# Kernel optimization log

Measured on AMD Instinct MI355X. Metric: run time of the kernel, lower is better.

The kernel has to match this reference:

```python
import jax, jax.numpy as jnp
import numpy as np

N, M, D = 1024, 1024, 256


def setup_inputs() -> dict:
    key = jax.random.key(0)
    k1, k2 = jax.random.split(key)
    z_x = jax.random.normal(k1, (N, D), dtype=jnp.float32)
    z_y = jax.random.normal(k2, (M, D), dtype=jnp.float32)
    return {"z_x": z_x, "z_y": z_y}


def reference(z_x, z_y):
    # s[i, j] = -sum_d |z_x[i, d] - z_y[j, d]|   -> [N, M] negative L1 distances
    s = -jnp.sum(jnp.abs(z_x[:, None, :] - z_y[None, :, :]), axis=-1)
    a = jax.nn.softmax(s, axis=1)  # row-wise alignment probs
    b = jax.nn.softmax(s, axis=0)  # column-wise alignment probs
    w = a + b - a * b              # soft symmetric alignment weights
    # weighted mean similarity (scalar)
    c = jnp.sum(w * s) / jnp.sum(w)
    return c
```

## Files before the change

### kernel.cpp

```cpp
#include <hip/hip_runtime.h>
#include <math.h>

#define NN 1024
#define MM 1024
#define DD 256
#define TI 32
#define TJ 64
#define NTI 32
#define NTJ 16
#define PITCH_H 264

typedef _Float16 f16x2 __attribute__((ext_vector_type(2)));
typedef _Float16 f16x4 __attribute__((ext_vector_type(4)));

__device__ inline f16x2 habs2(f16x2 v) {
  unsigned u = __builtin_bit_cast(unsigned, v) & 0x7FFF7FFFu;
  return __builtin_bit_cast(f16x2, u);
}

__device__ inline float dot2acc(f16x2 a, float acc) {
#if __has_builtin(__builtin_amdgcn_fdot2)
  const f16x2 one = {(_Float16)1.0f, (_Float16)1.0f};
  return __builtin_amdgcn_fdot2(a, one, acc, false);
#else
  return acc + (float)a.x + (float)a.y;
#endif
}

__device__ inline void merge_ms(float& m, float& s, float m2, float s2) {
  float mn = fmaxf(m, m2);
  s = s * __expf(m - mn) + s2 * __expf(m2 - mn);
  m = mn;
}

__device__ inline float wredSum(float v) {
#pragma unroll
  for (int o = 32; o > 0; o >>= 1) v += __shfl_down(v, o, 64);
  return v;
}

__global__ __launch_bounds__(256) void k_tile(const float* __restrict__ zx,
                                              const float* __restrict__ zy,
                                              float* __restrict__ S,
                                              float* __restrict__ rowPM,
                                              float* __restrict__ rowPS,
                                              float* __restrict__ colPM,
                                              float* __restrict__ colPS) {
  __shared__ __align__(16) _Float16 xs[TI * PITCH_H];
  __shared__ __align__(16) _Float16 ys[TJ * PITCH_H];
  __shared__ float lm[16][64];
  __shared__ float lsv[16][64];

  const int it = blockIdx.y, jt = blockIdx.x;
  const int i0 = it * TI, j0 = jt * TJ;
  const int t = threadIdx.x;
  const int tx = t & 15, ty = t >> 4;

#pragma unroll
  for (int k = 0; k < 8; ++k) {
    int idx4 = t + k * 256;
    int r = idx4 >> 6;
    int c4 = idx4 & 63;
    float4 v = reinterpret_cast<const float4*>(zx + (size_t)(i0 + r) * DD)[c4];
    f16x4 h = {(_Float16)v.x, (_Float16)v.y, (_Float16)v.z, (_Float16)v.w};
    *reinterpret_cast<f16x4*>(&xs[r * PITCH_H + c4 * 4]) = h;
  }
#pragma unroll
  for (int k = 0; k < 16; ++k) {
    int idx4 = t + k * 256;
    int r = idx4 >> 6;
    int c4 = idx4 & 63;
    float4 v = reinterpret_cast<const float4*>(zy + (size_t)(j0 + r) * DD)[c4];
    f16x4 h = {(_Float16)v.x, (_Float16)v.y, (_Float16)v.z, (_Float16)v.w};
    *reinterpret_cast<f16x4*>(&ys[r * PITCH_H + c4 * 4]) = h;
  }
  __syncthreads();

  float acc4[2][4] = {{0.f}};
  for (int s8 = 0; s8 < 32; ++s8) {
    uint4 xw[2], yw[4];
#pragma unroll
    for (int a = 0; a < 2; ++a)
      xw[a] = *reinterpret_cast<const uint4*>(&xs[(ty + a * 16) * PITCH_H + s8 * 8]);
#pragma unroll
    for (int b = 0; b < 4; ++b)
      yw[b] = *reinterpret_cast<const uint4*>(&ys[(tx + b * 16) * PITCH_H + s8 * 8]);
#pragma unroll
    for (int a = 0; a < 2; ++a)
#pragma unroll
      for (int b = 0; b < 4; ++b) {
        float acc = acc4[a][b];
        acc = dot2acc(habs2(__builtin_bit_cast(f16x2, xw[a].x) - __builtin_bit_cast(f16x2, yw[b].x)), acc);
        acc = dot2acc(habs2(__builtin_bit_cast(f16x2, xw[a].y) - __builtin_bit_cast(f16x2, yw[b].y)), acc);
        acc = dot2acc(habs2(__builtin_bit_cast(f16x2, xw[a].z) - __builtin_bit_cast(f16x2, yw[b].z)), acc);
        acc = dot2acc(habs2(__builtin_bit_cast(f16x2, xw[a].w) - __builtin_bit_cast(f16x2, yw[b].w)), acc);
        acc4[a][b] = acc;
      }
  }

#pragma unroll
  for (int a = 0; a < 2; ++a) {
    int i = i0 + ty + a * 16;
#pragma unroll
    for (int b = 0; b < 4; ++b) {
      int j = j0 + tx + b * 16;
      S[(size_t)i * MM + j] = -acc4[a][b];
    }
  }

#pragma unroll
  for (int a = 0; a < 2; ++a) {
    float m = -acc4[a][0];
#pragma unroll
    for (int b = 1; b < 4; ++b) m = fmaxf(m, -acc4[a][b]);
    float s = 0.f;
#pragma unroll
    for (int b = 0; b < 4; ++b) s += __expf(-acc4[a][b] - m);
#pragma unroll
    for (int off = 1; off < 16; off <<= 1) {
      float m2 = __shfl_xor(m, off, 64);
      float s2 = __shfl_xor(s, off, 64);
      merge_ms(m, s, m2, s2);
    }
    if (tx == 0) {
      int i = i0 + ty + a * 16;
      rowPM[(size_t)jt * NN + i] = m;
      rowPS[(size_t)jt * NN + i] = s;
    }
  }

#pragma unroll
  for (int b = 0; b < 4; ++b) {
    int c = tx + b * 16;
    float m = fmaxf(-acc4[0][b], -acc4[1][b]);
    float s = __expf(-acc4[0][b] - m) + __expf(-acc4[1][b] - m);
    lm[ty][c] = m;
    lsv[ty][c] = s;
  }
  __syncthreads();
  if (t < 64) {
    float m = lm[0][t], s = lsv[0][t];
#pragma unroll
    for (int k = 1; k < 16; ++k) merge_ms(m, s, lm[k][t], lsv[k][t]);
    colPM[(size_t)it * MM + j0 + t] = m;
    colPS[(size_t)it * MM + j0 + t] = s;
  }
}

__global__ __launch_bounds__(256) void k_merge(const float* __restrict__ rowPM,
                                               const float* __restrict__ rowPS,
                                               const float* __restrict__ colPM,
                                               const float* __restrict__ colPS,
                                               float* __restrict__ rowM,
                                               float* __restrict__ rowS,
                                               float* __restrict__ colM,
                                               float* __restrict__ colS) {
  int g = blockIdx.x * 256 + threadIdx.x;
  if (g < NN) {
    float m = rowPM[g], s = rowPS[g];
#pragma unroll
    for (int k = 1; k < NTJ; ++k)
      merge_ms(m, s, rowPM[(size_t)k * NN + g], rowPS[(size_t)k * NN + g]);
    rowM[g] = m;
    rowS[g] = s;
  } else {
    int c = g - NN;
    float m = colPM[c], s = colPS[c];
#pragma unroll
    for (int k = 1; k < NTI; ++k)
      merge_ms(m, s, colPM[(size_t)k * MM + c], colPS[(size_t)k * MM + c]);
    colM[c] = m;
    colS[c] = s;
  }
}

__global__ __launch_bounds__(256) void k_accum(const float* __restrict__ S,
                                               const float* __restrict__ rowM,
                                               const float* __restrict__ rowS,
                                               const float* __restrict__ colM,
                                               const float* __restrict__ colS,
                                               float* __restrict__ bNum,
                                               float* __restrict__ bDen) {
  const int i = blockIdx.x;
  const int t = threadIdx.x;
  float4 v = reinterpret_cast<const float4*>(S + (size_t)i * MM)[t];
  const float rm = rowM[i];
  const float rinv = 1.f / rowS[i];
  float4 cm = reinterpret_cast<const float4*>(colM)[t];
  float4 cs = reinterpret_cast<const float4*>(colS)[t];
  float num = 0.f, den = 0.f;
#define DO_COMP(VX, CMX, CSX)               \
  {                                         \
    float a = __expf((VX) - rm) * rinv;     \
    float b = __expf((VX) - (CMX)) / (CSX); \
    float w = a + b - a * b;                \
    num += w * (VX);                        \
    den += w;                               \
  }
  DO_COMP(v.x, cm.x, cs.x)
  DO_COMP(v.y, cm.y, cs.y)
  DO_COMP(v.z, cm.z, cs.z)
  DO_COMP(v.w, cm.w, cs.w)
#undef DO_COMP
  num = wredSum(num);
  den = wredSum(den);
  __shared__ float rn[4], rd[4];
  const int lane = t & 63, wv = t >> 6;
  if (lane == 0) { rn[wv] = num; rd[wv] = den; }
  __syncthreads();
  if (t == 0) {
    bNum[i] = rn[0] + rn[1] + rn[2] + rn[3];
    bDen[i] = rd[0] + rd[1] + rd[2] + rd[3];
  }
}

__global__ __launch_bounds__(256) void k_final(const float* __restrict__ bNum,
                                               const float* __restrict__ bDen,
                                               float* __restrict__ out) {
  const int t = threadIdx.x;
  float4 n4 = reinterpret_cast<const float4*>(bNum)[t];
  float4 d4 = reinterpret_cast<const float4*>(bDen)[t];
  float n = n4.x + n4.y + n4.z + n4.w;
  float d = d4.x + d4.y + d4.z + d4.w;
  n = wredSum(n);
  d = wredSum(d);
  __shared__ float rn[4], rd[4];
  const int lane = t & 63, wv = t >> 6;
  if (lane == 0) { rn[wv] = n; rd[wv] = d; }
  __syncthreads();
  if (t == 0) out[0] = (rn[0] + rn[1] + rn[2] + rn[3]) / (rd[0] + rd[1] + rd[2] + rd[3]);
}

extern "C" void kernel_launch(void* const* d_in, const int* in_sizes, int n_in,
                              void* d_out, int out_size, void* d_ws, size_t ws_size,
                              hipStream_t stream) {
  const float* zx = (const float*)d_in[0];
  const float* zy = (const float*)d_in[1];
  float* out = (float*)d_out;

  float* ws = (float*)d_ws;
  float* S     = ws;
  float* rowPM = S + (size_t)NN * MM;
  float* rowPS = rowPM + NTJ * NN;
  float* colPM = rowPS + NTJ * NN;
  float* colPS = colPM + NTI * MM;
  float* rowM  = colPS + NTI * MM;
  float* rowS  = rowM + NN;
  float* colM  = rowS + NN;
  float* colS  = colM + MM;
  float* bNum  = colS + MM;
  float* bDen  = bNum + NN;

  k_tile<<<dim3(NTJ, NTI), 256, 0, stream>>>(zx, zy, S, rowPM, rowPS, colPM, colPS);
  k_merge<<<8, 256, 0, stream>>>(rowPM, rowPS, colPM, colPS, rowM, rowS, colM, colS);
  k_accum<<<NN, 256, 0, stream>>>(S, rowM, rowS, colM, colS, bNum, bDen);
  k_final<<<1, 256, 0, stream>>>(bNum, bDen, out);
}
```

Measured before the change: 32.30 us.

## Fold merge and final reduction into tile and accum kernels via last-block atomics

Removes the separate merge and final-reduction kernels. The last tile block to finish a row or column strip, detected with atomic counters, now merges the partial max and sum statistics. The last accumulation block reduces the per-block sums to the scalar output. The accumulation kernel now handles four rows per block and precomputes the column reciprocals. This cuts two kernel launches and their gaps, at the cost of counters that are never reset (they rely on modular wraparound) and extra fences.

```diff
diff --git a/kernel.cpp b/kernel.cpp
--- a/kernel.cpp
+++ b/kernel.cpp
@@ -45,7 +45,13 @@
                                               float* __restrict__ rowPM,
                                               float* __restrict__ rowPS,
                                               float* __restrict__ colPM,
-                                              float* __restrict__ colPS) {
+                                              float* __restrict__ colPS,
+                                              float* __restrict__ rowM,
+                                              float* __restrict__ rowS,
+                                              float* __restrict__ colM,
+                                              float* __restrict__ colS,
+                                              unsigned* __restrict__ rowCtr,
+                                              unsigned* __restrict__ colCtr) {
   __shared__ __align__(16) _Float16 xs[TI * PITCH_H];
   __shared__ __align__(16) _Float16 ys[TJ * PITCH_H];
   __shared__ float lm[16][64];
@@ -145,32 +151,40 @@
     colPM[(size_t)it * MM + j0 + t] = m;
     colPS[(size_t)it * MM + j0 + t] = s;
   }
-}
-
-__global__ __launch_bounds__(256) void k_merge(const float* __restrict__ rowPM,
-                                               const float* __restrict__ rowPS,
-                                               const float* __restrict__ colPM,
-                                               const float* __restrict__ colPS,
-                                               float* __restrict__ rowM,
-                                               float* __restrict__ rowS,
-                                               float* __restrict__ colM,
-                                               float* __restrict__ colS) {
-  int g = blockIdx.x * 256 + threadIdx.x;
-  if (g < NN) {
-    float m = rowPM[g], s = rowPS[g];
-#pragma unroll
-    for (int k = 1; k < NTJ; ++k)
-      merge_ms(m, s, rowPM[(size_t)k * NN + g], rowPS[(size_t)k * NN + g]);
-    rowM[g] = m;
-    rowS[g] = s;
-  } else {
-    int c = g - NN;
-    float m = colPM[c], s = colPS[c];
-#pragma unroll
-    for (int k = 1; k < NTI; ++k)
-      merge_ms(m, s, colPM[(size_t)k * MM + c], colPS[(size_t)k * MM + c]);
-    colM[c] = m;
-    colS[c] = s;
+
+  __syncthreads();
+  __shared__ int doRow, doCol;
+  if (t == 0) {
+    __threadfence();
+    unsigned o1 = atomicAdd(&rowCtr[it], 1u);
+    doRow = ((o1 & (NTJ - 1u)) == (NTJ - 1u)) ? 1 : 0;
+    unsigned o2 = atomicAdd(&colCtr[jt], 1u);
+    doCol = ((o2 & (NTI - 1u)) == (NTI - 1u)) ? 1 : 0;
+  }
+  __syncthreads();
+  if (doRow) {
+    __threadfence();
+    if (t < TI) {
+      int i = i0 + t;
+      float m = rowPM[i], s = rowPS[i];
+#pragma unroll
+      for (int k = 1; k < NTJ; ++k)
+        merge_ms(m, s, rowPM[(size_t)k * NN + i], rowPS[(size_t)k * NN + i]);
+      rowM[i] = m;
+      rowS[i] = s;
+    }
+  }
+  if (doCol) {
+    __threadfence();
+    if (t < TJ) {
+      int j = j0 + t;
+      float m = colPM[j], s = colPS[j];
+#pragma unroll
+      for (int k = 1; k < NTI; ++k)
+        merge_ms(m, s, colPM[(size_t)k * MM + j], colPS[(size_t)k * MM + j]);
+      colM[j] = m;
+      colS[j] = s;
+    }
   }
 }
 
@@ -180,28 +194,46 @@
                                                const float* __restrict__ colM,
                                                const float* __restrict__ colS,
                                                float* __restrict__ bNum,
-                                               float* __restrict__ bDen) {
-  const int i = blockIdx.x;
+                                               float* __restrict__ bDen,
+                                               unsigned* __restrict__ accCtr,
+                                               float* __restrict__ out) {
+  const int bid = blockIdx.x;
   const int t = threadIdx.x;
-  float4 v = reinterpret_cast<const float4*>(S + (size_t)i * MM)[t];
-  const float rm = rowM[i];
-  const float rinv = 1.f / rowS[i];
+
   float4 cm = reinterpret_cast<const float4*>(colM)[t];
   float4 cs = reinterpret_cast<const float4*>(colS)[t];
+  float4 ci;
+  ci.x = 1.f / cs.x; ci.y = 1.f / cs.y; ci.z = 1.f / cs.z; ci.w = 1.f / cs.w;
+
+  __shared__ float rowMl[4], rowIl[4];
+  if (t < 4) {
+    int r = bid * 4 + t;
+    rowMl[t] = rowM[r];
+    rowIl[t] = 1.f / rowS[r];
+  }
+  __syncthreads();
+
   float num = 0.f, den = 0.f;
-#define DO_COMP(VX, CMX, CSX)               \
-  {                                         \
-    float a = __expf((VX) - rm) * rinv;     \
-    float b = __expf((VX) - (CMX)) / (CSX); \
-    float w = a + b - a * b;                \
-    num += w * (VX);                        \
-    den += w;                               \
-  }
-  DO_COMP(v.x, cm.x, cs.x)
-  DO_COMP(v.y, cm.y, cs.y)
-  DO_COMP(v.z, cm.z, cs.z)
-  DO_COMP(v.w, cm.w, cs.w)
+#pragma unroll
+  for (int rl = 0; rl < 4; ++rl) {
+    int row = bid * 4 + rl;
+    float4 v = reinterpret_cast<const float4*>(S + (size_t)row * MM)[t];
+    float rm = rowMl[rl], ri = rowIl[rl];
+#define DO_COMP(VX, CMX, CIX)                 \
+    {                                         \
+      float a = __expf((VX) - rm) * ri;       \
+      float b = __expf((VX) - (CMX)) * (CIX); \
+      float w = a + b - a * b;                \
+      num += w * (VX);                        \
+      den += w;                               \
+    }
+    DO_COMP(v.x, cm.x, ci.x)
+    DO_COMP(v.y, cm.y, ci.y)
+    DO_COMP(v.z, cm.z, ci.z)
+    DO_COMP(v.w, cm.w, ci.w)
 #undef DO_COMP
+  }
+
   num = wredSum(num);
   den = wredSum(den);
   __shared__ float rn[4], rd[4];
@@ -209,26 +241,27 @@
   if (lane == 0) { rn[wv] = num; rd[wv] = den; }
   __syncthreads();
   if (t == 0) {
-    bNum[i] = rn[0] + rn[1] + rn[2] + rn[3];
-    bDen[i] = rd[0] + rd[1] + rd[2] + rd[3];
-  }
-}
-
-__global__ __launch_bounds__(256) void k_final(const float* __restrict__ bNum,
-                                               const float* __restrict__ bDen,
-                                               float* __restrict__ out) {
-  const int t = threadIdx.x;
-  float4 n4 = reinterpret_cast<const float4*>(bNum)[t];
-  float4 d4 = reinterpret_cast<const float4*>(bDen)[t];
-  float n = n4.x + n4.y + n4.z + n4.w;
-  float d = d4.x + d4.y + d4.z + d4.w;
-  n = wredSum(n);
-  d = wredSum(d);
-  __shared__ float rn[4], rd[4];
-  const int lane = t & 63, wv = t >> 6;
-  if (lane == 0) { rn[wv] = n; rd[wv] = d; }
-  __syncthreads();
-  if (t == 0) out[0] = (rn[0] + rn[1] + rn[2] + rn[3]) / (rd[0] + rd[1] + rd[2] + rd[3]);
+    bNum[bid] = rn[0] + rn[1] + rn[2] + rn[3];
+    bDen[bid] = rd[0] + rd[1] + rd[2] + rd[3];
+  }
+
+  __shared__ int isLast;
+  if (t == 0) {
+    __threadfence();
+    unsigned old = atomicAdd(accCtr, 1u);
+    isLast = ((old & 255u) == 255u) ? 1 : 0;
+  }
+  __syncthreads();
+  if (isLast) {
+    __threadfence();
+    float n = bNum[t];
+    float d = bDen[t];
+    n = wredSum(n);
+    d = wredSum(d);
+    if (lane == 0) { rn[wv] = n; rd[wv] = d; }
+    __syncthreads();
+    if (t == 0) out[0] = (rn[0] + rn[1] + rn[2] + rn[3]) / (rd[0] + rd[1] + rd[2] + rd[3]);
+  }
 }
 
 extern "C" void kernel_launch(void* const* d_in, const int* in_sizes, int n_in,
@@ -249,10 +282,12 @@
   float* colM  = rowS + NN;
   float* colS  = colM + MM;
   float* bNum  = colS + MM;
-  float* bDen  = bNum + NN;
-
-  k_tile<<<dim3(NTJ, NTI), 256, 0, stream>>>(zx, zy, S, rowPM, rowPS, colPM, colPS);
-  k_merge<<<8, 256, 0, stream>>>(rowPM, rowPS, colPM, colPS, rowM, rowS, colM, colS);
-  k_accum<<<NN, 256, 0, stream>>>(S, rowM, rowS, colM, colS, bNum, bDen);
-  k_final<<<1, 256, 0, stream>>>(bNum, bDen, out);
-}
+  float* bDen  = bNum + 256;
+  unsigned* rowCtr = (unsigned*)(bDen + 256);
+  unsigned* colCtr = rowCtr + NTI;
+  unsigned* accCtr = colCtr + NTJ;
+
+  k_tile<<<dim3(NTJ, NTI), 256, 0, stream>>>(zx, zy, S, rowPM, rowPS, colPM, colPS,
+                                             rowM, rowS, colM, colS, rowCtr, colCtr);
+  k_accum<<<256, 256, 0, stream>>>(S, rowM, rowS, colM, colS, bNum, bDen, accCtr, out);
+}
```

Result: slower. 49.04 us (+51.8%).
